# Optimization experiments

Measured on AMD Instinct MI355X. Metric: run time of the kernel, lower is better.

Reference implementation:

```python
import jax, jax.numpy as jnp
import numpy as np

MARGIN = 1.0
EPS = 1e-12


def setup_inputs() -> dict:
    key = jax.random.key(0)
    k1, k2, k3 = jax.random.split(key, 3)
    B, C, D = 16384, 500, 512
    features = jax.random.normal(k1, (B, D), dtype=jnp.float32)
    prototypes = jax.random.normal(k2, (C, D), dtype=jnp.float32)
    labels = jax.random.randint(k3, (B,), 0, C, dtype=jnp.int64)
    return {"features": features, "prototypes": prototypes, "labels": labels}


def reference(features, prototypes, labels):
    # Pairwise L2 distances [B, C] via the expanded form (no [B,C,D] intermediate)
    f2 = jnp.sum(features * features, axis=-1, keepdims=True)   # [B, 1]
    p2 = jnp.sum(prototypes * prototypes, axis=-1)               # [C]
    sq = f2 + p2 - 2.0 * (features @ prototypes.T)               # [B, C]
    dists = jnp.sqrt(jnp.maximum(sq, EPS))                       # [B, C]

    B, C = dists.shape
    d_pos = jnp.take_along_axis(dists, labels[:, None], axis=1)[:, 0]  # [B]
    pos_mask = jax.nn.one_hot(labels, C, dtype=bool)             # [B, C]
    d_neg_min = jnp.min(jnp.where(pos_mask, jnp.inf, dists), axis=-1)  # [B]

    loss = jnp.mean(jax.nn.relu(d_pos - d_neg_min + MARGIN))
    return loss
```

## Files before the change

kernel.cpp:

```cpp
#include <hip/hip_runtime.h>
#include <stdint.h>
#include <stddef.h>

#define BB 16384
#define CC 500
#define DD 512
#define PADC 512
#define LMARGIN 1.0f
#define EPSQ 1e-12f

#define GROUP_P 32
#define N_GROUPS (PADC / GROUP_P)
#define ROWB 1040

typedef __attribute__((ext_vector_type(8))) _Float16 f16x8;
typedef __attribute__((ext_vector_type(4))) float f32x4;

#define GLOBAL_AS __attribute__((address_space(1)))
#define LDS_AS __attribute__((address_space(3)))

__device__ __forceinline__ void ld_lds16(const void* g, void* l) {
  __builtin_amdgcn_global_load_lds((const GLOBAL_AS void*)g, (LDS_AS void*)l, 16, 0, 0);
}

__device__ __forceinline__ unsigned short f2h_bits(float f) {
  union { _Float16 h; unsigned short u; } v;
  v.h = (_Float16)f;
  return v.u;
}

__global__ void prep_kernel(const float* __restrict__ protos,
                            unsigned short* __restrict__ protoH,
                            float* __restrict__ p2) {
  int c = blockIdx.x;
  int t = threadIdx.x;
  float v0 = 0.f, v1 = 0.f;
  if (c < CC) {
    v0 = protos[c * DD + 2 * t];
    v1 = protos[c * DD + 2 * t + 1];
  }
  unsigned pk = (unsigned)f2h_bits(v0) | ((unsigned)f2h_bits(v1) << 16);
  ((unsigned*)protoH)[c * (DD / 2) + t] = pk;
  float s = v0 * v0 + v1 * v1;
#pragma unroll
  for (int d = 1; d < 64; d <<= 1) s += __shfl_xor(s, d, 64);
  __shared__ float ws4[4];
  if ((t & 63) == 0) ws4[t >> 6] = s;
  __syncthreads();
  if (t == 0) p2[c] = ws4[0] + ws4[1] + ws4[2] + ws4[3];
}

__launch_bounds__(256, 1)
__global__ void loss_kernel(const float* __restrict__ feat,
                            const int* __restrict__ labels,
                            const unsigned short* __restrict__ protoH,
                            const float* __restrict__ p2,
                            float* __restrict__ out) {
  __shared__ __align__(16) unsigned char ldsB[GROUP_P * ROWB];
  __shared__ float f2s[4][16];
  __shared__ float wsum[4];

  const int tid = threadIdx.x;
  const int wave = tid >> 6;
  const int lane = tid & 63;
  const int lane16 = lane & 15;
  const int quad = lane >> 4;
  const int rowBase = blockIdx.x * 64 + wave * 16;

#pragma unroll
  for (int r = 0; r < 8; ++r) {
    int p = wave * 8 + r;
    ld_lds16(protoH + (size_t)p * DD + lane * 8, ldsB + p * ROWB);
  }

  f16x8 afrag[16];
  float f2part = 0.f;
  const float* frow = feat + (size_t)(rowBase + lane16) * DD;
#pragma unroll
  for (int s = 0; s < 16; ++s) {
    const int k0 = s * 32 + quad * 8;
    f32x4 a0 = *(const f32x4*)(frow + k0);
    f32x4 a1 = *(const f32x4*)(frow + k0 + 4);
    f16x8 af;
#pragma unroll
    for (int j = 0; j < 4; ++j) {
      af[j] = (_Float16)a0[j];
      af[j + 4] = (_Float16)a1[j];
      f2part = fmaf(a0[j], a0[j], f2part);
      f2part = fmaf(a1[j], a1[j], f2part);
    }
    afrag[s] = af;
  }
  f2part += __shfl_xor(f2part, 16, 64);
  f2part += __shfl_xor(f2part, 32, 64);
  if (quad == 0) f2s[wave][lane16] = f2part;

  int lab[4];
#pragma unroll
  for (int i = 0; i < 4; ++i) lab[i] = labels[rowBase + quad * 4 + i];

  __syncthreads();

  float f2r[4];
#pragma unroll
  for (int i = 0; i < 4; ++i) f2r[i] = f2s[wave][quad * 4 + i];

  float runMin[4], posD[4];
#pragma unroll
  for (int i = 0; i < 4; ++i) { runMin[i] = 1e30f; posD[i] = -1e30f; }

  for (int g = 0; g < N_GROUPS; ++g) {
    f32x4 acc0 = {0.f, 0.f, 0.f, 0.f};
    f32x4 acc1 = {0.f, 0.f, 0.f, 0.f};
    const unsigned char* bbase = ldsB + lane16 * ROWB + quad * 16;
#pragma unroll
    for (int s = 0; s < 16; ++s) {
      f16x8 b0 = *(const f16x8*)(bbase + s * 64);
      f16x8 b1 = *(const f16x8*)(bbase + 16 * ROWB + s * 64);
      acc0 = __builtin_amdgcn_mfma_f32_16x16x32_f16(afrag[s], b0, acc0, 0, 0, 0);
      acc1 = __builtin_amdgcn_mfma_f32_16x16x32_f16(afrag[s], b1, acc1, 0, 0, 0);
    }
    __syncthreads();
    if (g + 1 < N_GROUPS) {
#pragma unroll
      for (int r = 0; r < 8; ++r) {
        int p = wave * 8 + r;
        ld_lds16(protoH + (size_t)((g + 1) * GROUP_P + p) * DD + lane * 8,
                 ldsB + p * ROWB);
      }
    }
    const int col0 = g * GROUP_P + lane16;
    const int col1 = col0 + 16;
    const float p20 = p2[col0];
    const float p21 = p2[col1];
#pragma unroll
    for (int i = 0; i < 4; ++i) {
      float d0 = sqrtf(fmaxf(f2r[i] + p20 - 2.f * acc0[i], EPSQ));
      float d1 = sqrtf(fmaxf(f2r[i] + p21 - 2.f * acc1[i], EPSQ));
      bool isPos0 = (col0 == lab[i]);
      bool isPos1 = (col1 == lab[i]);
      posD[i] = fmaxf(posD[i], isPos0 ? d0 : -1e30f);
      posD[i] = fmaxf(posD[i], isPos1 ? d1 : -1e30f);
      runMin[i] = fminf(runMin[i], (!isPos0 && col0 < CC) ? d0 : 1e30f);
      runMin[i] = fminf(runMin[i], (!isPos1 && col1 < CC) ? d1 : 1e30f);
    }
    __syncthreads();
  }

  float termSum = 0.f;
#pragma unroll
  for (int i = 0; i < 4; ++i) {
    float m = runMin[i], p = posD[i];
#pragma unroll
    for (int d = 1; d < 16; d <<= 1) {
      m = fminf(m, __shfl_xor(m, d, 64));
      p = fmaxf(p, __shfl_xor(p, d, 64));
    }
    termSum += fmaxf(p - m + LMARGIN, 0.f);
  }
  float contrib = (lane16 == 0) ? termSum : 0.f;
#pragma unroll
  for (int d = 1; d < 64; d <<= 1) contrib += __shfl_xor(contrib, d, 64);
  if (lane == 0) wsum[wave] = contrib;
  __syncthreads();
  if (tid == 0)
    atomicAdd(out, (wsum[0] + wsum[1] + wsum[2] + wsum[3]) * (1.0f / BB));
}

extern "C" void kernel_launch(void* const* d_in, const int* in_sizes, int n_in,
                              void* d_out, int out_size, void* d_ws, size_t ws_size,
                              hipStream_t stream) {
  const float* feat = (const float*)d_in[0];
  const float* protos = (const float*)d_in[1];
  const int* labels = (const int*)d_in[2];
  float* out = (float*)d_out;

  unsigned short* protoH = (unsigned short*)d_ws;
  float* p2 = (float*)((char*)d_ws + (size_t)PADC * DD * sizeof(unsigned short));

  hipMemsetAsync(d_out, 0, sizeof(float) * (out_size > 0 ? out_size : 1), stream);
  prep_kernel<<<PADC, 256, 0, stream>>>(protos, protoH, p2);
  loss_kernel<<<BB / 64, 256, 0, stream>>>(feat, labels, protoH, p2, out);
}
```

Before: 107.9 us.

## Split prototype columns across 8 waves with a triple-buffered K-quarter LDS ring

Result: slower. 120.6 us (+11.8%).

```diff
diff --git a/kernel.cpp b/kernel.cpp
--- a/kernel.cpp
+++ b/kernel.cpp
@@ -9,9 +9,13 @@
 #define LMARGIN 1.0f
 #define EPSQ 1e-12f
 
-#define GROUP_P 32
-#define N_GROUPS (PADC / GROUP_P)
-#define ROWB 1040
+#define ROWS_PER_BLOCK 64
+#define NG 8
+#define NKQ 4
+#define NIT (NG * NKQ)
+#define QUADB 1056
+#define UNITB (4 * QUADB)
+#define NRING 3
 
 typedef __attribute__((ext_vector_type(8))) _Float16 f16x8;
 typedef __attribute__((ext_vector_type(4))) float f32x4;
@@ -31,9 +35,11 @@
 
 __global__ void prep_kernel(const float* __restrict__ protos,
                             unsigned short* __restrict__ protoH,
-                            float* __restrict__ p2) {
+                            float* __restrict__ p2,
+                            float* __restrict__ out) {
   int c = blockIdx.x;
   int t = threadIdx.x;
+  if (c == 0 && t == 0) out[0] = 0.f;
   float v0 = 0.f, v1 = 0.f;
   if (c < CC) {
     v0 = protos[c * DD + 2 * t];
@@ -50,121 +56,174 @@
   if (t == 0) p2[c] = ws4[0] + ws4[1] + ws4[2] + ws4[3];
 }
 
-__launch_bounds__(256, 1)
+__launch_bounds__(512, 2)
 __global__ void loss_kernel(const float* __restrict__ feat,
                             const int* __restrict__ labels,
                             const unsigned short* __restrict__ protoH,
                             const float* __restrict__ p2,
                             float* __restrict__ out) {
-  __shared__ __align__(16) unsigned char ldsB[GROUP_P * ROWB];
-  __shared__ float f2s[4][16];
-  __shared__ float wsum[4];
+  __shared__ __align__(16) unsigned char ldsB[4 * NRING * UNITB];
+  __shared__ float p2s[PADC];
+  __shared__ float f2s[ROWS_PER_BLOCK];
+  __shared__ float redMin[4][ROWS_PER_BLOCK];
+  __shared__ float redPos[4][ROWS_PER_BLOCK];
 
   const int tid = threadIdx.x;
-  const int wave = tid >> 6;
+  const int w = tid >> 6;
   const int lane = tid & 63;
   const int lane16 = lane & 15;
   const int quad = lane >> 4;
-  const int rowBase = blockIdx.x * 64 + wave * 16;
-
-#pragma unroll
-  for (int r = 0; r < 8; ++r) {
-    int p = wave * 8 + r;
-    ld_lds16(protoH + (size_t)p * DD + lane * 8, ldsB + p * ROWB);
-  }
-
-  f16x8 afrag[16];
-  float f2part = 0.f;
-  const float* frow = feat + (size_t)(rowBase + lane16) * DD;
-#pragma unroll
-  for (int s = 0; s < 16; ++s) {
-    const int k0 = s * 32 + quad * 8;
-    f32x4 a0 = *(const f32x4*)(frow + k0);
-    f32x4 a1 = *(const f32x4*)(frow + k0 + 4);
-    f16x8 af;
-#pragma unroll
-    for (int j = 0; j < 4; ++j) {
-      af[j] = (_Float16)a0[j];
-      af[j + 4] = (_Float16)a1[j];
-      f2part = fmaf(a0[j], a0[j], f2part);
-      f2part = fmaf(a1[j], a1[j], f2part);
-    }
-    afrag[s] = af;
-  }
-  f2part += __shfl_xor(f2part, 16, 64);
-  f2part += __shfl_xor(f2part, 32, 64);
-  if (quad == 0) f2s[wave][lane16] = f2part;
-
-  int lab[4];
-#pragma unroll
-  for (int i = 0; i < 4; ++i) lab[i] = labels[rowBase + quad * 4 + i];
-
+  const int mtile = w & 1;
+  const int cq = w >> 1;
+  const int rowBase = blockIdx.x * ROWS_PER_BLOCK + mtile * 32;
+
+  {
+    const int g = 0, kq = 0;
+#pragma unroll
+    for (int jj = 0; jj < 2; ++jj) {
+      int j = 2 * mtile + jj;
+      int r = 4 * j + (lane >> 4);
+      const unsigned short* src = protoH +
+          (size_t)(cq * 128 + g * 16 + r) * DD + kq * 128 + (lane & 15) * 8;
+      ld_lds16(src, ldsB + (cq * NRING + 0) * UNITB + j * QUADB);
+    }
+  }
+
+  p2s[tid] = p2[tid];
+
+  f16x8 afrag[2][16];
+  float f2part[2] = {0.f, 0.f};
+#pragma unroll
+  for (int t = 0; t < 2; ++t) {
+    const float* frow = feat + (size_t)(rowBase + t * 16 + lane16) * DD;
+#pragma unroll
+    for (int j = 0; j < 16; ++j) {
+      const int k0 = j * 32 + quad * 8;
+      f32x4 a0 = *(const f32x4*)(frow + k0);
+      f32x4 a1 = *(const f32x4*)(frow + k0 + 4);
+      f16x8 af;
+#pragma unroll
+      for (int u = 0; u < 4; ++u) {
+        af[u] = (_Float16)a0[u];
+        af[u + 4] = (_Float16)a1[u];
+        f2part[t] = fmaf(a0[u], a0[u], f2part[t]);
+        f2part[t] = fmaf(a1[u], a1[u], f2part[t]);
+      }
+      afrag[t][j] = af;
+    }
+    f2part[t] += __shfl_xor(f2part[t], 16, 64);
+    f2part[t] += __shfl_xor(f2part[t], 32, 64);
+    if (quad == 0) f2s[mtile * 32 + t * 16 + lane16] = f2part[t];
+  }
+
+  int lab[2][4];
+#pragma unroll
+  for (int t = 0; t < 2; ++t)
+#pragma unroll
+    for (int i = 0; i < 4; ++i)
+      lab[t][i] = labels[rowBase + t * 16 + quad * 4 + i];
+
+  f32x4 acc[2][2];
+#pragma unroll
+  for (int t = 0; t < 2; ++t)
+#pragma unroll
+    for (int h = 0; h < 2; ++h)
+      acc[t][h] = (f32x4){0.f, 0.f, 0.f, 0.f};
+
+  float runMin[2][4], posD[2][4];
+#pragma unroll
+  for (int t = 0; t < 2; ++t)
+#pragma unroll
+    for (int i = 0; i < 4; ++i) { runMin[t][i] = 1e30f; posD[t][i] = -1e30f; }
+
+  float f2r[2][4];
+
+  int ring = 0;
+  for (int it = 0; it < NIT; ++it) {
+    __syncthreads();
+
+    const int ringNext = (ring + 1 == NRING) ? 0 : ring + 1;
+    if (it + 1 < NIT) {
+      const int it1 = it + 1;
+      const int g1 = it1 >> 2, kq1 = it1 & 3;
+#pragma unroll
+      for (int jj = 0; jj < 2; ++jj) {
+        int j = 2 * mtile + jj;
+        int r = 4 * j + (lane >> 4);
+        const unsigned short* src = protoH +
+            (size_t)(cq * 128 + g1 * 16 + r) * DD + kq1 * 128 + (lane & 15) * 8;
+        ld_lds16(src, ldsB + (cq * NRING + ringNext) * UNITB + j * QUADB);
+      }
+    }
+
+    const int g = it >> 2, kq = it & 3;
+    const unsigned char* base = ldsB + (cq * NRING + ring) * UNITB +
+                                (lane16 >> 2) * QUADB + (lane16 & 3) * 256 +
+                                quad * 16;
+#pragma unroll
+    for (int s = 0; s < 4; ++s) {
+      f16x8 b = *(const f16x8*)(base + s * 64);
+      acc[0][s & 1] = __builtin_amdgcn_mfma_f32_16x16x32_f16(afrag[0][kq * 4 + s], b, acc[0][s & 1], 0, 0, 0);
+      acc[1][s & 1] = __builtin_amdgcn_mfma_f32_16x16x32_f16(afrag[1][kq * 4 + s], b, acc[1][s & 1], 0, 0, 0);
+    }
+
+    if (kq == 3) {
+      if (it == 3) {
+#pragma unroll
+        for (int t = 0; t < 2; ++t)
+#pragma unroll
+          for (int i = 0; i < 4; ++i)
+            f2r[t][i] = f2s[mtile * 32 + t * 16 + quad * 4 + i];
+      }
+      const int col = cq * 128 + g * 16 + lane16;
+      const float p2c = p2s[col];
+      const bool colOk = (col < CC);
+#pragma unroll
+      for (int t = 0; t < 2; ++t) {
+#pragma unroll
+        for (int i = 0; i < 4; ++i) {
+          float dot = acc[t][0][i] + acc[t][1][i];
+          float d = sqrtf(fmaxf(f2r[t][i] + p2c - 2.f * dot, EPSQ));
+          bool isPos = (col == lab[t][i]);
+          posD[t][i] = fmaxf(posD[t][i], isPos ? d : -1e30f);
+          runMin[t][i] = fminf(runMin[t][i], (!isPos && colOk) ? d : 1e30f);
+        }
+#pragma unroll
+        for (int h = 0; h < 2; ++h) acc[t][h] = (f32x4){0.f, 0.f, 0.f, 0.f};
+      }
+    }
+    ring = ringNext;
+  }
+
+#pragma unroll
+  for (int t = 0; t < 2; ++t) {
+#pragma unroll
+    for (int i = 0; i < 4; ++i) {
+      float m = runMin[t][i], p = posD[t][i];
+#pragma unroll
+      for (int d = 1; d < 16; d <<= 1) {
+        m = fminf(m, __shfl_xor(m, d, 64));
+        p = fmaxf(p, __shfl_xor(p, d, 64));
+      }
+      if (lane16 == 0) {
+        int r = mtile * 32 + t * 16 + quad * 4 + i;
+        redMin[cq][r] = m;
+        redPos[cq][r] = p;
+      }
+    }
+  }
   __syncthreads();
 
-  float f2r[4];
-#pragma unroll
-  for (int i = 0; i < 4; ++i) f2r[i] = f2s[wave][quad * 4 + i];
-
-  float runMin[4], posD[4];
-#pragma unroll
-  for (int i = 0; i < 4; ++i) { runMin[i] = 1e30f; posD[i] = -1e30f; }
-
-  for (int g = 0; g < N_GROUPS; ++g) {
-    f32x4 acc0 = {0.f, 0.f, 0.f, 0.f};
-    f32x4 acc1 = {0.f, 0.f, 0.f, 0.f};
-    const unsigned char* bbase = ldsB + lane16 * ROWB + quad * 16;
-#pragma unroll
-    for (int s = 0; s < 16; ++s) {
-      f16x8 b0 = *(const f16x8*)(bbase + s * 64);
-      f16x8 b1 = *(const f16x8*)(bbase + 16 * ROWB + s * 64);
-      acc0 = __builtin_amdgcn_mfma_f32_16x16x32_f16(afrag[s], b0, acc0, 0, 0, 0);
-      acc1 = __builtin_amdgcn_mfma_f32_16x16x32_f16(afrag[s], b1, acc1, 0, 0, 0);
-    }
-    __syncthreads();
-    if (g + 1 < N_GROUPS) {
-#pragma unroll
-      for (int r = 0; r < 8; ++r) {
-        int p = wave * 8 + r;
-        ld_lds16(protoH + (size_t)((g + 1) * GROUP_P + p) * DD + lane * 8,
-                 ldsB + p * ROWB);
-      }
-    }
-    const int col0 = g * GROUP_P + lane16;
-    const int col1 = col0 + 16;
-    const float p20 = p2[col0];
-    const float p21 = p2[col1];
-#pragma unroll
-    for (int i = 0; i < 4; ++i) {
-      float d0 = sqrtf(fmaxf(f2r[i] + p20 - 2.f * acc0[i], EPSQ));
-      float d1 = sqrtf(fmaxf(f2r[i] + p21 - 2.f * acc1[i], EPSQ));
-      bool isPos0 = (col0 == lab[i]);
-      bool isPos1 = (col1 == lab[i]);
-      posD[i] = fmaxf(posD[i], isPos0 ? d0 : -1e30f);
-      posD[i] = fmaxf(posD[i], isPos1 ? d1 : -1e30f);
-      runMin[i] = fminf(runMin[i], (!isPos0 && col0 < CC) ? d0 : 1e30f);
-      runMin[i] = fminf(runMin[i], (!isPos1 && col1 < CC) ? d1 : 1e30f);
-    }
-    __syncthreads();
-  }
-
-  float termSum = 0.f;
-#pragma unroll
-  for (int i = 0; i < 4; ++i) {
-    float m = runMin[i], p = posD[i];
-#pragma unroll
-    for (int d = 1; d < 16; d <<= 1) {
-      m = fminf(m, __shfl_xor(m, d, 64));
-      p = fmaxf(p, __shfl_xor(p, d, 64));
-    }
-    termSum += fmaxf(p - m + LMARGIN, 0.f);
-  }
-  float contrib = (lane16 == 0) ? termSum : 0.f;
-#pragma unroll
-  for (int d = 1; d < 64; d <<= 1) contrib += __shfl_xor(contrib, d, 64);
-  if (lane == 0) wsum[wave] = contrib;
-  __syncthreads();
-  if (tid == 0)
-    atomicAdd(out, (wsum[0] + wsum[1] + wsum[2] + wsum[3]) * (1.0f / BB));
+  if (tid < 64) {
+    float m = fminf(fminf(redMin[0][tid], redMin[1][tid]),
+                    fminf(redMin[2][tid], redMin[3][tid]));
+    float p = fmaxf(fmaxf(redPos[0][tid], redPos[1][tid]),
+                    fmaxf(redPos[2][tid], redPos[3][tid]));
+    float term = fmaxf(p - m + LMARGIN, 0.f);
+#pragma unroll
+    for (int d = 1; d < 64; d <<= 1) term += __shfl_xor(term, d, 64);
+    if (tid == 0) atomicAdd(out, term * (1.0f / BB));
+  }
 }
 
 extern "C" void kernel_launch(void* const* d_in, const int* in_sizes, int n_in,
@@ -178,7 +237,6 @@
   unsigned short* protoH = (unsigned short*)d_ws;
   float* p2 = (float*)((char*)d_ws + (size_t)PADC * DD * sizeof(unsigned short));
 
-  hipMemsetAsync(d_out, 0, sizeof(float) * (out_size > 0 ? out_size : 1), stream);
-  prep_kernel<<<PADC, 256, 0, stream>>>(protos, protoH, p2);
-  loss_kernel<<<BB / 64, 256, 0, stream>>>(feat, labels, protoH, p2, out);
-}
+  prep_kernel<<<PADC, 256, 0, stream>>>(protos, protoH, p2, out);
+  loss_kernel<<<BB / ROWS_PER_BLOCK, 512, 0, stream>>>(feat, labels, protoH, p2, out);
+}
```
